# Kernel optimization log

Measured on AMD Instinct MI355X. Metric: run time of the kernel, lower is better.

The kernel has to match this reference:

```python
import jax, jax.numpy as jnp
import numpy as np

TOP_K = 2
ROUTE_SCALE = 1.0
EPS = 1e-20

B, S, D = 2, 512, 1024
E = 8            # num_experts
F = 768          # moe_intermediate_size
FS = 768 * 1     # shared expert intermediate (moe_intermediate_size * num_shared_experts)


def setup_inputs() -> dict:
    key = jax.random.key(0)
    ks = jax.random.split(key, 9)
    s = 0.02
    return {
        "hidden_states": jax.random.normal(ks[0], (B, S, D), dtype=jnp.float32),
        "W_gate_router": jax.random.normal(ks[1], (D, E), dtype=jnp.float32) * s,
        "expert_bias": jnp.zeros((E,), dtype=jnp.float32),
        "Wg": jax.random.normal(ks[2], (E, D, F), dtype=jnp.float32) * s,
        "Wu": jax.random.normal(ks[3], (E, D, F), dtype=jnp.float32) * s,
        "Wd": jax.random.normal(ks[4], (E, F, D), dtype=jnp.float32) * s,
        "Wg_s": jax.random.normal(ks[5], (D, FS), dtype=jnp.float32) * s,
        "Wu_s": jax.random.normal(ks[6], (D, FS), dtype=jnp.float32) * s,
        "Wd_s": jax.random.normal(ks[7], (FS, D), dtype=jnp.float32) * s,
    }


def reference(hidden_states, W_gate_router, expert_bias, Wg, Wu, Wd, Wg_s, Wu_s, Wd_s):
    b, s, d = hidden_states.shape
    x = hidden_states.reshape(-1, d)                      # [T, D]
    T = x.shape[0]

    # ---- token-choice top-k router (sigmoid scoring, route_norm) ----
    logits = x @ W_gate_router                            # [T, E]
    scores = jax.nn.sigmoid(logits.astype(jnp.float32))   # [T, E] fp32
    _, sel = jax.lax.top_k(scores + expert_bias, TOP_K)   # [T, K] (bias only for selection)
    top_scores = jnp.take_along_axis(scores, sel, axis=1)  # [T, K]
    top_scores = top_scores / (top_scores.sum(-1, keepdims=True) + EPS)  # route_norm
    top_scores = top_scores * ROUTE_SCALE

    # ---- shared expert (always active) ----
    shared = (jax.nn.silu(x @ Wg_s) * (x @ Wu_s)) @ Wd_s  # [T, D]

    # ---- dispatch: N = T*K routed slots (scatter-add is order-independent,
    #      so the torch stable-argsort grouping is mathematically a no-op) ----
    tok = jnp.repeat(jnp.arange(T), TOP_K)                # [N] source token per slot
    exp = sel.reshape(-1)                                 # [N] expert per slot
    w = top_scores.reshape(-1)                            # [N]
    xr = x[tok]                                           # [N, D]

    # per-expert SiLU-GLU MLP, vectorized over experts then select own expert's row
    h = jax.nn.silu(jnp.einsum('nd,edf->enf', xr, Wg)) * jnp.einsum('nd,edf->enf', xr, Wu)
    out_all = jnp.einsum('enf,efd->end', h, Wd)           # [E, N, D]
    routed = out_all[exp, jnp.arange(exp.shape[0])]       # [N, D]
    routed = (routed.astype(jnp.float32) * w[:, None]).astype(hidden_states.dtype)

    # ---- combine: scatter-add routed outputs onto shared output ----
    out = shared.at[tok].add(routed)                      # [T, D]
    return out.reshape(b, s, d)
```

## Files before the change

### kernel.cpp

```cpp
#include <hip/hip_runtime.h>
#include <hip/hip_bf16.h>
#include <math.h>

#define T_TOK   1024
#define D_DIM   1024
#define E_NUM   8
#define F_DIM   768
#define N_SLOTS 2048

typedef unsigned short u16;
typedef __attribute__((ext_vector_type(8))) short bf16x8;
typedef __attribute__((ext_vector_type(4))) float f32x4;

#define WS_SEL    0
#define WS_WTS    8192
#define WS_BUCKET 16384
#define WS_COUNTS 49152
#define WS_OFFS   49216
#define WS_POS    49280
#define WS_XB     65536
#define WS_H      (WS_XB + 2097152)
#define WS_WDT    (WS_H + 4718592)
#define WS_WDST   (WS_WDT + 12582912)
#define WS_WGUT   (WS_WDST + 1572864)
#define WS_WGUST  (WS_WGUT + 25165824)
#define WS_Y      WS_WGUT

__device__ __forceinline__ u16 f2bf(float x) {
    unsigned int u = __float_as_uint(x);
    u += 0x7fffu + ((u >> 16) & 1u);
    return (u16)(u >> 16);
}
__device__ __forceinline__ float bf2f(u16 h) {
    return __uint_as_float(((unsigned int)h) << 16);
}

__device__ __forceinline__ void async16(const void* g, void* s) {
    __builtin_amdgcn_global_load_lds(
        (const __attribute__((address_space(1))) unsigned int*)g,
        (__attribute__((address_space(3))) unsigned int*)s, 16, 0, 0);
}

#define PIN()   __builtin_amdgcn_sched_barrier(0)
#define BAR()   do { PIN(); __builtin_amdgcn_s_barrier(); PIN(); } while (0)
#define WAIT6() do { asm volatile("s_waitcnt vmcnt(6)" ::: "memory"); PIN(); } while (0)
#define WAIT0() do { asm volatile("s_waitcnt vmcnt(0)" ::: "memory"); PIN(); } while (0)

__device__ __forceinline__ void tr_tile(
    const float* __restrict__ src, u16* __restrict__ dst,
    int R, int C, int r0, int c0, u16 (*tile)[72])
{
    int t = threadIdx.x;
    int rr = t >> 4, cq = (t & 15) * 4;
#pragma unroll
    for (int i = 0; i < 4; ++i) {
        int rl = rr + 16 * i;
        float4 v = *(const float4*)(src + (size_t)(r0 + rl) * C + c0 + cq);
        tile[cq + 0][rl] = f2bf(v.x);
        tile[cq + 1][rl] = f2bf(v.y);
        tile[cq + 2][rl] = f2bf(v.z);
        tile[cq + 3][rl] = f2bf(v.w);
    }
    __syncthreads();
#pragma unroll
    for (int j = 0; j < 2; ++j) {
        int idx = t + 256 * j;
        int cc = idx >> 3, q = idx & 7;
        *(uint4*)(dst + (size_t)(c0 + cc) * R + r0 + q * 8) = *(const uint4*)&tile[cc][q * 8];
    }
}

__global__ __launch_bounds__(256) void prep1_kernel(
    const float* __restrict__ X, const float* __restrict__ Wr,
    const float* __restrict__ bias,
    const float* __restrict__ Wg, const float* __restrict__ Wu,
    const float* __restrict__ Wgs, const float* __restrict__ Wus,
    u16* __restrict__ Xb, int* __restrict__ sel, float* __restrict__ wts,
    u16* __restrict__ Wgut, u16* __restrict__ Wgust)
{
    const int i = blockIdx.x;
    if (i < 3456) {
        __shared__ u16 tile[64][72];
        const int z = i / 192;
        const int rem = i - z * 192;
        const int rtile = rem / 12, ctile = rem - rtile * 12;
        const float* src; u16* dst;
        if (z < 8)       { src = Wg + (size_t)z * D_DIM * F_DIM;       dst = Wgut + (size_t)z * 1536 * D_DIM; }
        else if (z < 16) { src = Wu + (size_t)(z - 8) * D_DIM * F_DIM; dst = Wgut + (size_t)(z - 8) * 1536 * D_DIM + (size_t)F_DIM * D_DIM; }
        else if (z == 16){ src = Wgs; dst = Wgust; }
        else             { src = Wus; dst = Wgust + (size_t)F_DIM * D_DIM; }
        tr_tile(src, dst, D_DIM, F_DIM, rtile * 64, ctile * 64, tile);
        return;
    }
    int t = (i - 3456) * 4 + (threadIdx.x >> 6);
    int lane = threadIdx.x & 63;
    const float* xrow = X + (size_t)t * D_DIM;
    u16* brow = Xb + (size_t)t * D_DIM;
    float acc[E_NUM];
#pragma unroll
    for (int e = 0; e < E_NUM; ++e) acc[e] = 0.f;
#pragma unroll
    for (int q = 0; q < 4; ++q) {
        int d = q * 256 + lane * 4;
        float4 v = *(const float4*)(xrow + d);
        ushort4 o;
        o.x = f2bf(v.x); o.y = f2bf(v.y); o.z = f2bf(v.z); o.w = f2bf(v.w);
        *(ushort4*)(brow + d) = o;
        const float xv[4] = {v.x, v.y, v.z, v.w};
#pragma unroll
        for (int jj = 0; jj < 4; ++jj) {
            const float4* wr = (const float4*)(Wr + (size_t)(d + jj) * E_NUM);
            float4 w0 = wr[0], w1 = wr[1];
            acc[0] += xv[jj] * w0.x; acc[1] += xv[jj] * w0.y;
            acc[2] += xv[jj] * w0.z; acc[3] += xv[jj] * w0.w;
            acc[4] += xv[jj] * w1.x; acc[5] += xv[jj] * w1.y;
            acc[6] += xv[jj] * w1.z; acc[7] += xv[jj] * w1.w;
        }
    }
#pragma unroll
    for (int e = 0; e < E_NUM; ++e)
#pragma unroll
        for (int off = 32; off > 0; off >>= 1)
            acc[e] += __shfl_xor(acc[e], off);
    if (lane == 0) {
        float s[E_NUM], b[E_NUM];
#pragma unroll
        for (int e = 0; e < E_NUM; ++e) {
            s[e] = 1.f / (1.f + expf(-acc[e]));
            b[e] = s[e] + bias[e];
        }
        int i1 = 0; float b1 = b[0];
#pragma unroll
        for (int e = 1; e < E_NUM; ++e) if (b[e] > b1) { b1 = b[e]; i1 = e; }
        int i2 = -1; float b2 = -INFINITY;
#pragma unroll
        for (int e = 0; e < E_NUM; ++e) {
            if (e == i1) continue;
            if (b[e] > b2) { b2 = b[e]; i2 = e; }
        }
        float s1 = s[i1], s2 = s[i2];
        float denom = s1 + s2 + 1e-20f;
        sel[2 * t] = i1; sel[2 * t + 1] = i2;
        wts[2 * t] = s1 / denom; wts[2 * t + 1] = s2 / denom;
    }
}

__global__ __launch_bounds__(512) void dispatch_kernel(
    const int* __restrict__ sel, int* __restrict__ bucket,
    int* __restrict__ counts, int* __restrict__ offs, int* __restrict__ pos)
{
    __shared__ int soffs[E_NUM + 1];
    int e = threadIdx.x >> 6;
    int lane = threadIdx.x & 63;
    int running = 0;
    for (int base = 0; base < N_SLOTS; base += 64) {
        int slot = base + lane;
        bool mine = (sel[slot] == e);
        unsigned long long mask = __ballot(mine);
        if (mine) {
            int rank = running + __popcll(mask & ((1ull << lane) - 1ull));
            bucket[e * T_TOK + rank] = slot;
        }
        running += __popcll(mask);
    }
    if (lane == 0) counts[e] = running;
    __syncthreads();
    if (threadIdx.x == 0) {
        int o = 0;
        for (int k = 0; k < E_NUM; ++k) { soffs[k] = o; offs[k] = o; o += counts[k]; }
        soffs[E_NUM] = o; offs[E_NUM] = o;
    }
    __syncthreads();
    int base_off = soffs[e];
    for (int r = lane; r < running; r += 64)
        pos[bucket[e * T_TOK + r]] = base_off + r;
}

__global__ __launch_bounds__(256, 3) void proj1_fused(
    const u16* __restrict__ Xb, const u16* __restrict__ Wgut, const u16* __restrict__ Wgust,
    u16* __restrict__ H,
    const int* __restrict__ bucket, const int* __restrict__ counts, const int* __restrict__ offs,
    const float* __restrict__ Wd, const float* __restrict__ Wds,
    u16* __restrict__ Wdt, u16* __restrict__ Wdst)
{
    __shared__ u16 smem[2][192 * 64];
    const int i = blockIdx.x;
    if (i >= 3584) {
        const int j = i - 3584;
        const int z = j / 192;
        const int rem = j - z * 192;
        const int rtile = rem >> 4, ctile = rem & 15;
        const float* src; u16* dst;
        if (z < 8) { src = Wd + (size_t)z * F_DIM * D_DIM; dst = Wdt + (size_t)z * D_DIM * F_DIM; }
        else       { src = Wds; dst = Wdst; }
        tr_tile(src, dst, F_DIM, D_DIM, rtile * 64, ctile * 64, (u16(*)[72])&smem[0][0]);
        return;
    }

    const int cxcd = i & 7, m = i >> 3;
    const int y = m & 31, phi = m >> 5;
    const int panel = phi * 8 + cxcd;
    if (panel >= 108) return;
    const int unit = panel / 12, x = panel - unit * 12;

    int nrows, rbase; const u16* Wt;
    if (unit < E_NUM) {
        nrows = counts[unit]; rbase = offs[unit];
        Wt = Wgut + (size_t)unit * 1536 * D_DIM;
    } else {
        nrows = T_TOK; rbase = N_SLOTS; Wt = Wgust;
    }
    const int row0 = y * 64;
    if (row0 >= nrows) return;

    const int t = threadIdx.x;
    const int wv = t >> 6, lane = t & 63, l15 = lane & 15, lg = lane >> 4;
    const int wm = wv >> 1, wn = wv & 1;
    const int rl = lane >> 3, cch = lane & 7;

    const u16* srcA[2];
#pragma unroll
    for (int j = 0; j < 2; ++j) {
        int arow = wv * 16 + j * 8 + rl;
        int grow = min(row0 + arow, nrows - 1);
        if (unit < E_NUM) grow = bucket[unit * T_TOK + grow] >> 1;
        srcA[j] = Xb + (size_t)grow * D_DIM + (cch ^ (arow & 7)) * 8;
    }
    const u16* srcB[4];
#pragma unroll
    for (int j = 0; j < 4; ++j) {
        int br = wv * 32 + j * 8 + rl;
        size_t n = (size_t)(br >> 6) * F_DIM + x * 64 + (br & 63);
        srcB[j] = Wt + n * D_DIM + (cch ^ (br & 7)) * 8;
    }

    f32x4 accg[2][2], accu[2][2];
    const f32x4 z4 = {0.f, 0.f, 0.f, 0.f};
#pragma unroll
    for (int ri = 0; ri < 2; ++ri)
#pragma unroll
        for (int ci = 0; ci < 2; ++ci) { accg[ri][ci] = z4; accu[ri][ci] = z4; }

#define STAGE1(buf, kt) do { \
    _Pragma("unroll") \
    for (int j = 0; j < 2; ++j) \
        async16(srcA[j] + (kt), &smem[buf][(wv * 16 + j * 8) * 64]); \
    _Pragma("unroll") \
    for (int j = 0; j < 4; ++j) \
        async16(srcB[j] + (kt), &smem[buf][(64 + wv * 32 + j * 8) * 64]); \
} while (0)

#define COMP1(buf) do { \
    bf16x8 av[2][2], bg[2][2], bu[2][2]; \
    _Pragma("unroll") \
    for (int ri = 0; ri < 2; ++ri) { \
        int row = wm * 32 + ri * 16 + l15; \
        _Pragma("unroll") \
        for (int kk = 0; kk < 2; ++kk) { \
            int ch = ((kk << 2) | lg) ^ (row & 7); \
            av[ri][kk] = *(const bf16x8*)&smem[buf][row * 64 + ch * 8]; \
        } \
    } \
    _Pragma("unroll") \
    for (int ci = 0; ci < 2; ++ci) { \
        int br = wn * 32 + ci * 16 + l15; \
        _Pragma("unroll") \
        for (int kk = 0; kk < 2; ++kk) { \
            int ch = ((kk << 2) | lg) ^ (br & 7); \
            bg[ci][kk] = *(const bf16x8*)&smem[buf][(64 + br) * 64 + ch * 8]; \
            bu[ci][kk] = *(const bf16x8*)&smem[buf][(128 + br) * 64 + ch * 8]; \
        } \
    } \
    _Pragma("unroll") \
    for (int kk = 0; kk < 2; ++kk) \
        _Pragma("unroll") \
        for (int ri = 0; ri < 2; ++ri) \
            _Pragma("unroll") \
            for (int ci = 0; ci < 2; ++ci) { \
                accg[ri][ci] = __builtin_amdgcn_mfma_f32_16x16x32_bf16( \
                    av[ri][kk], bg[ci][kk], accg[ri][ci], 0, 0, 0); \
                accu[ri][ci] = __builtin_amdgcn_mfma_f32_16x16x32_bf16( \
                    av[ri][kk], bu[ci][kk], accu[ri][ci], 0, 0, 0); \
            } \
} while (0)

    STAGE1(0, 0);
    for (int tt = 0; tt < 16; tt += 2) {
        STAGE1(1, (tt + 1) * 64);
        WAIT6();
        BAR();
        COMP1(0);
        BAR();
        if (tt + 2 < 16) { STAGE1(0, (tt + 2) * 64); WAIT6(); }
        else             { WAIT0(); }
        BAR();
        COMP1(1);
        BAR();
    }
#undef STAGE1
#undef COMP1

#pragma unroll
    for (int ri = 0; ri < 2; ++ri)
#pragma unroll
        for (int ci = 0; ci < 2; ++ci) {
            int n = x * 64 + wn * 32 + ci * 16 + l15;
#pragma unroll
            for (int r = 0; r < 4; ++r) {
                int row = row0 + wm * 32 + ri * 16 + lg * 4 + r;
                if (row >= nrows) continue;
                float gv = accg[ri][ci][r];
                float uv = accu[ri][ci][r];
                H[(size_t)(rbase + row) * F_DIM + n] =
                    f2bf(gv / (1.f + __expf(-gv)) * uv);
            }
        }
}

__global__ __launch_bounds__(256, 3) void proj2(
    const u16* __restrict__ H, const u16* __restrict__ Wdt, const u16* __restrict__ Wdst,
    float* __restrict__ Y,
    const int* __restrict__ counts, const int* __restrict__ offs)
{
    const int i = blockIdx.x;
    const int cxcd = i & 7, m = i >> 3;
    const int y = m & 31, phi = m >> 5;
    const int panel = phi * 8 + cxcd;
    const int unit = panel >> 3, x = panel & 7;

    int nrows, rbase; const u16* Wt;
    if (unit < E_NUM) {
        nrows = counts[unit]; rbase = offs[unit];
        Wt = Wdt + (size_t)unit * D_DIM * F_DIM;
    } else {
        nrows = T_TOK; rbase = N_SLOTS; Wt = Wdst;
    }
    const int row0 = y * 64, n0 = x * 128;
    if (row0 >= nrows) return;

    __shared__ u16 smem[2][192 * 64];

    const int t = threadIdx.x;
    const int wv = t >> 6, lane = t & 63, l15 = lane & 15, lg = lane >> 4;
    const int wm = wv >> 1, wn = wv & 1;
    const int rl = lane >> 3, cch = lane & 7;

    const u16* srcA[2];
#pragma unroll
    for (int j = 0; j < 2; ++j) {
        int arow = wv * 16 + j * 8 + rl;
        int grow = rbase + min(row0 + arow, nrows - 1);
        srcA[j] = H + (size_t)grow * F_DIM + (cch ^ (arow & 7)) * 8;
    }
    const u16* srcB[4];
#pragma unroll
    for (int j = 0; j < 4; ++j) {
        int br = wv * 32 + j * 8 + rl;
        srcB[j] = Wt + (size_t)(n0 + br) * F_DIM + (cch ^ (br & 7)) * 8;
    }

    f32x4 acc[2][4];
    const f32x4 z4 = {0.f, 0.f, 0.f, 0.f};
#pragma unroll
    for (int ri = 0; ri < 2; ++ri)
#pragma unroll
        for (int ci = 0; ci < 4; ++ci) acc[ri][ci] = z4;

#define STAGE2(buf, kt) do { \
    _Pragma("unroll") \
    for (int j = 0; j < 2; ++j) \
        async16(srcA[j] + (kt), &smem[buf][(wv * 16 + j * 8) * 64]); \
    _Pragma("unroll") \
    for (int j = 0; j < 4; ++j) \
        async16(srcB[j] + (kt), &smem[buf][(64 + wv * 32 + j * 8) * 64]); \
} while (0)

#define COMP2(buf) do { \
    bf16x8 av[2][2], bv[4][2]; \
    _Pragma("unroll") \
    for (int ri = 0; ri < 2; ++ri) { \
        int row = wm * 32 + ri * 16 + l15; \
        _Pragma("unroll") \
        for (int kk = 0; kk < 2; ++kk) { \
            int ch = ((kk << 2) | lg) ^ (row & 7); \
            av[ri][kk] = *(const bf16x8*)&smem[buf][row * 64 + ch * 8]; \
        } \
    } \
    _Pragma("unroll") \
    for (int ci = 0; ci < 4; ++ci) { \
        int br = wn * 64 + ci * 16 + l15; \
        _Pragma("unroll") \
        for (int kk = 0; kk < 2; ++kk) { \
            int ch = ((kk << 2) | lg) ^ (br & 7); \
            bv[ci][kk] = *(const bf16x8*)&smem[buf][(64 + br) * 64 + ch * 8]; \
        } \
    } \
    _Pragma("unroll") \
    for (int kk = 0; kk < 2; ++kk) \
        _Pragma("unroll") \
        for (int ri = 0; ri < 2; ++ri) \
            _Pragma("unroll") \
            for (int ci = 0; ci < 4; ++ci) \
                acc[ri][ci] = __builtin_amdgcn_mfma_f32_16x16x32_bf16( \
                    av[ri][kk], bv[ci][kk], acc[ri][ci], 0, 0, 0); \
} while (0)

    STAGE2(0, 0);
    for (int tt = 0; tt < 12; tt += 2) {
        STAGE2(1, (tt + 1) * 64);
        WAIT6();
        BAR();
        COMP2(0);
        BAR();
        if (tt + 2 < 12) { STAGE2(0, (tt + 2) * 64); WAIT6(); }
        else             { WAIT0(); }
        BAR();
        COMP2(1);
        BAR();
    }
#undef STAGE2
#undef COMP2

#pragma unroll
    for (int ri = 0; ri < 2; ++ri)
#pragma unroll
        for (int ci = 0; ci < 4; ++ci) {
            int n = n0 + wn * 64 + ci * 16 + l15;
#pragma unroll
            for (int r = 0; r < 4; ++r) {
                int row = row0 + wm * 32 + ri * 16 + lg * 4 + r;
                if (row >= nrows) continue;
                Y[(size_t)(rbase + row) * D_DIM + n] = acc[ri][ci][r];
            }
        }
}

__global__ __launch_bounds__(256) void combine_kernel(
    const float* __restrict__ Y, const int* __restrict__ pos,
    const float* __restrict__ wts, float* __restrict__ out)
{
    int t = blockIdx.x;
    int d = threadIdx.x * 4;
    int p0 = pos[2 * t], p1 = pos[2 * t + 1];
    float w0 = wts[2 * t], w1 = wts[2 * t + 1];
    float4 a = *(const float4*)(Y + (size_t)(N_SLOTS + t) * D_DIM + d);
    float4 b = *(const float4*)(Y + (size_t)p0 * D_DIM + d);
    float4 cc = *(const float4*)(Y + (size_t)p1 * D_DIM + d);
    float4 o;
    o.x = a.x + w0 * b.x + w1 * cc.x;
    o.y = a.y + w0 * b.y + w1 * cc.y;
    o.z = a.z + w0 * b.z + w1 * cc.z;
    o.w = a.w + w0 * b.w + w1 * cc.w;
    *(float4*)(out + (size_t)t * D_DIM + d) = o;
}

extern "C" void kernel_launch(void* const* d_in, const int* in_sizes, int n_in,
                              void* d_out, int out_size, void* d_ws, size_t ws_size,
                              hipStream_t stream) {
    const float* X    = (const float*)d_in[0];
    const float* Wr   = (const float*)d_in[1];
    const float* bias = (const float*)d_in[2];
    const float* Wg   = (const float*)d_in[3];
    const float* Wu   = (const float*)d_in[4];
    const float* Wd   = (const float*)d_in[5];
    const float* Wgs  = (const float*)d_in[6];
    const float* Wus  = (const float*)d_in[7];
    const float* Wds  = (const float*)d_in[8];
    float* out = (float*)d_out;

    char* ws = (char*)d_ws;
    int*   sel    = (int*)(ws + WS_SEL);
    float* wtsv   = (float*)(ws + WS_WTS);
    int*   bucket = (int*)(ws + WS_BUCKET);
    int*   counts = (int*)(ws + WS_COUNTS);
    int*   offs   = (int*)(ws + WS_OFFS);
    int*   pos    = (int*)(ws + WS_POS);
    u16*   Xb     = (u16*)(ws + WS_XB);
    u16*   H      = (u16*)(ws + WS_H);
    u16*   Wdt    = (u16*)(ws + WS_WDT);
    u16*   Wdst   = (u16*)(ws + WS_WDST);
    u16*   Wgut   = (u16*)(ws + WS_WGUT);
    u16*   Wgust  = (u16*)(ws + WS_WGUST);
    float* Y      = (float*)(ws + WS_Y);

    prep1_kernel<<<3712, 256, 0, stream>>>(
        X, Wr, bias, Wg, Wu, Wgs, Wus, Xb, sel, wtsv, Wgut, Wgust);
    dispatch_kernel<<<1, 512, 0, stream>>>(sel, bucket, counts, offs, pos);

    proj1_fused<<<5312, 256, 0, stream>>>(
        Xb, Wgut, Wgust, H, bucket, counts, offs, Wd, Wds, Wdt, Wdst);
    proj2<<<2304, 256, 0, stream>>>(H, Wdt, Wdst, Y, counts, offs);
    combine_kernel<<<T_TOK, 256, 0, stream>>>(Y, pos, wtsv, out);
}
```

Measured before the change: 87.03 us.

## Read fp32 Wd directly in proj2, converting to bf16 in registers

Removes the separate transpose/convert pass for the down-projection weights that used to run inside proj1. proj2 now loads fp32 Wd columns through registers, packs them to bf16 and writes them into swizzled LDS, with a 64-column tile and register-prefetch double buffering. The proj1 and proj2 grids are resized so rows are tiled by 16 rather than 32. This saves one full read-convert-write of Wd to workspace, but proj2 now reads twice the bytes of weight data with strided scalar loads, and its inner loop uses synchronous loads instead of async LDS copies.

```diff
diff --git a/kernel.cpp b/kernel.cpp
--- a/kernel.cpp
+++ b/kernel.cpp
@@ -9,6 +9,7 @@
 #define N_SLOTS 2048
 
 typedef unsigned short u16;
+typedef unsigned int   u32;
 typedef __attribute__((ext_vector_type(8))) short bf16x8;
 typedef __attribute__((ext_vector_type(4))) float f32x4;
 
@@ -20,20 +21,16 @@
 #define WS_POS    49280
 #define WS_XB     65536
 #define WS_H      (WS_XB + 2097152)
-#define WS_WDT    (WS_H + 4718592)
-#define WS_WDST   (WS_WDT + 12582912)
-#define WS_WGUT   (WS_WDST + 1572864)
+#define WS_Y      (WS_H + 4718592)
+#define WS_WGUT   (WS_Y + 12582912)
 #define WS_WGUST  (WS_WGUT + 25165824)
-#define WS_Y      WS_WGUT
 
 __device__ __forceinline__ u16 f2bf(float x) {
-    unsigned int u = __float_as_uint(x);
+    u32 u = __float_as_uint(x);
     u += 0x7fffu + ((u >> 16) & 1u);
     return (u16)(u >> 16);
 }
-__device__ __forceinline__ float bf2f(u16 h) {
-    return __uint_as_float(((unsigned int)h) << 16);
-}
+#define PKBF(hi, lo) __builtin_amdgcn_perm(__float_as_uint(hi), __float_as_uint(lo), 0x07060302u)
 
 __device__ __forceinline__ void async16(const void* g, void* s) {
     __builtin_amdgcn_global_load_lds(
@@ -176,29 +173,14 @@
         pos[bucket[e * T_TOK + r]] = base_off + r;
 }
 
-__global__ __launch_bounds__(256, 3) void proj1_fused(
+__global__ __launch_bounds__(256, 3) void proj1(
     const u16* __restrict__ Xb, const u16* __restrict__ Wgut, const u16* __restrict__ Wgust,
     u16* __restrict__ H,
-    const int* __restrict__ bucket, const int* __restrict__ counts, const int* __restrict__ offs,
-    const float* __restrict__ Wd, const float* __restrict__ Wds,
-    u16* __restrict__ Wdt, u16* __restrict__ Wdst)
-{
-    __shared__ u16 smem[2][192 * 64];
+    const int* __restrict__ bucket, const int* __restrict__ counts, const int* __restrict__ offs)
+{
     const int i = blockIdx.x;
-    if (i >= 3584) {
-        const int j = i - 3584;
-        const int z = j / 192;
-        const int rem = j - z * 192;
-        const int rtile = rem >> 4, ctile = rem & 15;
-        const float* src; u16* dst;
-        if (z < 8) { src = Wd + (size_t)z * F_DIM * D_DIM; dst = Wdt + (size_t)z * D_DIM * F_DIM; }
-        else       { src = Wds; dst = Wdst; }
-        tr_tile(src, dst, F_DIM, D_DIM, rtile * 64, ctile * 64, (u16(*)[72])&smem[0][0]);
-        return;
-    }
-
     const int cxcd = i & 7, m = i >> 3;
-    const int y = m & 31, phi = m >> 5;
+    const int y = m & 15, phi = m >> 4;
     const int panel = phi * 8 + cxcd;
     if (panel >= 108) return;
     const int unit = panel / 12, x = panel - unit * 12;
@@ -212,6 +194,8 @@
     }
     const int row0 = y * 64;
     if (row0 >= nrows) return;
+
+    __shared__ u16 smem[2][192 * 64];
 
     const int t = threadIdx.x;
     const int wv = t >> 6, lane = t & 63, l15 = lane & 15, lg = lane >> 4;
@@ -318,117 +302,112 @@
 }
 
 __global__ __launch_bounds__(256, 3) void proj2(
-    const u16* __restrict__ H, const u16* __restrict__ Wdt, const u16* __restrict__ Wdst,
+    const u16* __restrict__ H,
+    const float* __restrict__ Wd, const float* __restrict__ Wds,
     float* __restrict__ Y,
     const int* __restrict__ counts, const int* __restrict__ offs)
 {
     const int i = blockIdx.x;
     const int cxcd = i & 7, m = i >> 3;
-    const int y = m & 31, phi = m >> 5;
+    const int y = m & 15, phi = m >> 4;
     const int panel = phi * 8 + cxcd;
-    const int unit = panel >> 3, x = panel & 7;
-
-    int nrows, rbase; const u16* Wt;
+    if (panel >= 144) return;
+    const int unit = panel >> 4, x = panel & 15;
+
+    int nrows, rbase; const float* Bm;
     if (unit < E_NUM) {
         nrows = counts[unit]; rbase = offs[unit];
-        Wt = Wdt + (size_t)unit * D_DIM * F_DIM;
-    } else {
-        nrows = T_TOK; rbase = N_SLOTS; Wt = Wdst;
-    }
-    const int row0 = y * 64, n0 = x * 128;
+        Bm = Wd + (size_t)unit * F_DIM * D_DIM;
+    } else { nrows = T_TOK; rbase = N_SLOTS; Bm = Wds; }
+    const int row0 = y * 64;
     if (row0 >= nrows) return;
 
-    __shared__ u16 smem[2][192 * 64];
+    __shared__ u16 smem[2][128 * 64];
 
     const int t = threadIdx.x;
-    const int wv = t >> 6, lane = t & 63, l15 = lane & 15, lg = lane >> 4;
+    const int wv = t >> 6, lane = t & 63, l15 = lane & 15, g = lane >> 4;
     const int wm = wv >> 1, wn = wv & 1;
-    const int rl = lane >> 3, cch = lane & 7;
-
-    const u16* srcA[2];
-#pragma unroll
-    for (int j = 0; j < 2; ++j) {
-        int arow = wv * 16 + j * 8 + rl;
-        int grow = rbase + min(row0 + arow, nrows - 1);
-        srcA[j] = H + (size_t)grow * F_DIM + (cch ^ (arow & 7)) * 8;
-    }
-    const u16* srcB[4];
-#pragma unroll
-    for (int j = 0; j < 4; ++j) {
-        int br = wv * 32 + j * 8 + rl;
-        srcB[j] = Wt + (size_t)(n0 + br) * F_DIM + (cch ^ (br & 7)) * 8;
-    }
-
-    f32x4 acc[2][4];
+
+    const int ar = t >> 2, ac = t & 3;
+    const int grow = rbase + min(row0 + ar, nrows - 1);
+    const u16* srcA = H + (size_t)grow * F_DIM + ac * 8;
+    const int wA0 = ar * 64 + ((ac     ^ (ar & 7)) * 8);
+    const int wA1 = ar * 64 + (((ac+4) ^ (ar & 7)) * 8);
+
+    const int bn = t & 63;
+    const int bq = t >> 6;
+    const float* srcB = Bm + (size_t)(bq * 16) * D_DIM + x * 64 + bn;
+    int wB[2];
+#pragma unroll
+    for (int q = 0; q < 2; ++q)
+        wB[q] = (64 + bn) * 64 + (((bq * 2 + q) ^ (bn & 7)) * 8);
+
+    f32x4 acc[2][2];
     const f32x4 z4 = {0.f, 0.f, 0.f, 0.f};
 #pragma unroll
     for (int ri = 0; ri < 2; ++ri)
 #pragma unroll
-        for (int ci = 0; ci < 4; ++ci) acc[ri][ci] = z4;
-
-#define STAGE2(buf, kt) do { \
-    _Pragma("unroll") \
-    for (int j = 0; j < 2; ++j) \
-        async16(srcA[j] + (kt), &smem[buf][(wv * 16 + j * 8) * 64]); \
-    _Pragma("unroll") \
-    for (int j = 0; j < 4; ++j) \
-        async16(srcB[j] + (kt), &smem[buf][(64 + wv * 32 + j * 8) * 64]); \
+        for (int ci = 0; ci < 2; ++ci) acc[ri][ci] = z4;
+
+    uint4 pa0, pa1;
+    float pb[16];
+#define LOAD2(kt) do { \
+    pa0 = *(const uint4*)(srcA + (kt)); \
+    pa1 = *(const uint4*)(srcA + (kt) + 32); \
+    const float* _bp = srcB + (size_t)(kt) * D_DIM; \
+    _Pragma("unroll") \
+    for (int ii = 0; ii < 16; ++ii) pb[ii] = _bp[(size_t)ii * D_DIM]; \
 } while (0)
-
+#define WRITE2(buf) do { \
+    *(uint4*)&smem[buf][wA0] = pa0; \
+    *(uint4*)&smem[buf][wA1] = pa1; \
+    _Pragma("unroll") \
+    for (int q = 0; q < 2; ++q) { \
+        u32 pk[4]; \
+        _Pragma("unroll") \
+        for (int j = 0; j < 4; ++j) pk[j] = PKBF(pb[8*q + 2*j + 1], pb[8*q + 2*j]); \
+        *(uint4*)&smem[buf][wB[q]] = *(const uint4*)pk; \
+    } \
+} while (0)
 #define COMP2(buf) do { \
-    bf16x8 av[2][2], bv[4][2]; \
-    _Pragma("unroll") \
-    for (int ri = 0; ri < 2; ++ri) { \
-        int row = wm * 32 + ri * 16 + l15; \
-        _Pragma("unroll") \
-        for (int kk = 0; kk < 2; ++kk) { \
-            int ch = ((kk << 2) | lg) ^ (row & 7); \
-            av[ri][kk] = *(const bf16x8*)&smem[buf][row * 64 + ch * 8]; \
-        } \
-    } \
-    _Pragma("unroll") \
-    for (int ci = 0; ci < 4; ++ci) { \
-        int br = wn * 64 + ci * 16 + l15; \
-        _Pragma("unroll") \
-        for (int kk = 0; kk < 2; ++kk) { \
-            int ch = ((kk << 2) | lg) ^ (br & 7); \
-            bv[ci][kk] = *(const bf16x8*)&smem[buf][(64 + br) * 64 + ch * 8]; \
-        } \
-    } \
-    _Pragma("unroll") \
-    for (int kk = 0; kk < 2; ++kk) \
+    const u16* _p = smem[buf]; \
+    _Pragma("unroll") \
+    for (int kk = 0; kk < 2; ++kk) { \
+        const int ch = (((kk << 2) | g) ^ (l15 & 7)) * 8; \
+        bf16x8 _a[2], _b[2]; \
+        _Pragma("unroll") \
+        for (int ri = 0; ri < 2; ++ri) \
+            _a[ri] = *(const bf16x8*)&_p[(wm * 32 + ri * 16 + l15) * 64 + ch]; \
+        _Pragma("unroll") \
+        for (int ci = 0; ci < 2; ++ci) \
+            _b[ci] = *(const bf16x8*)&_p[(64 + wn * 32 + ci * 16 + l15) * 64 + ch]; \
         _Pragma("unroll") \
         for (int ri = 0; ri < 2; ++ri) \
             _Pragma("unroll") \
-            for (int ci = 0; ci < 4; ++ci) \
-                acc[ri][ci] = __builtin_amdgcn_mfma_f32_16x16x32_bf16( \
-                    av[ri][kk], bv[ci][kk], acc[ri][ci], 0, 0, 0); \
+            for (int ci = 0; ci < 2; ++ci) \
+                acc[ri][ci] = __builtin_amdgcn_mfma_f32_16x16x32_bf16(_a[ri], _b[ci], acc[ri][ci], 0, 0, 0); \
+    } \
 } while (0)
 
-    STAGE2(0, 0);
-    for (int tt = 0; tt < 12; tt += 2) {
-        STAGE2(1, (tt + 1) * 64);
-        WAIT6();
-        BAR();
-        COMP2(0);
-        BAR();
-        if (tt + 2 < 12) { STAGE2(0, (tt + 2) * 64); WAIT6(); }
-        else             { WAIT0(); }
-        BAR();
-        COMP2(1);
-        BAR();
-    }
-#undef STAGE2
+    LOAD2(0);
+    for (int tt = 0; tt < 12; ++tt) {
+        WRITE2(tt & 1);
+        if (tt + 1 < 12) LOAD2((tt + 1) * 64);
+        __syncthreads();
+        COMP2(tt & 1);
+    }
+#undef LOAD2
+#undef WRITE2
 #undef COMP2
 
 #pragma unroll
     for (int ri = 0; ri < 2; ++ri)
 #pragma unroll
-        for (int ci = 0; ci < 4; ++ci) {
-            int n = n0 + wn * 64 + ci * 16 + l15;
+        for (int ci = 0; ci < 2; ++ci) {
+            int n = x * 64 + wn * 32 + ci * 16 + l15;
 #pragma unroll
             for (int r = 0; r < 4; ++r) {
-                int row = row0 + wm * 32 + ri * 16 + lg * 4 + r;
+                int row = row0 + wm * 32 + ri * 16 + g * 4 + r;
                 if (row >= nrows) continue;
                 Y[(size_t)(rbase + row) * D_DIM + n] = acc[ri][ci][r];
             }
@@ -477,18 +456,15 @@
     int*   pos    = (int*)(ws + WS_POS);
     u16*   Xb     = (u16*)(ws + WS_XB);
     u16*   H      = (u16*)(ws + WS_H);
-    u16*   Wdt    = (u16*)(ws + WS_WDT);
-    u16*   Wdst   = (u16*)(ws + WS_WDST);
+    float* Y      = (float*)(ws + WS_Y);
     u16*   Wgut   = (u16*)(ws + WS_WGUT);
     u16*   Wgust  = (u16*)(ws + WS_WGUST);
-    float* Y      = (float*)(ws + WS_Y);
 
     prep1_kernel<<<3712, 256, 0, stream>>>(
         X, Wr, bias, Wg, Wu, Wgs, Wus, Xb, sel, wtsv, Wgut, Wgust);
     dispatch_kernel<<<1, 512, 0, stream>>>(sel, bucket, counts, offs, pos);
 
-    proj1_fused<<<5312, 256, 0, stream>>>(
-        Xb, Wgut, Wgust, H, bucket, counts, offs, Wd, Wds, Wdt, Wdst);
-    proj2<<<2304, 256, 0, stream>>>(H, Wdt, Wdst, Y, counts, offs);
+    proj1<<<1792, 256, 0, stream>>>(Xb, Wgut, Wgust, H, bucket, counts, offs);
+    proj2<<<2304, 256, 0, stream>>>(H, Wd, Wds, Y, counts, offs);
     combine_kernel<<<T_TOK, 256, 0, stream>>>(Y, pos, wtsv, out);
 }
```

Measured after the change: 81.64 us. 6.2% less time.
